# Kernel tuning notes

Hardware: AMD Instinct MI355X
Metric: run time of the kernel (lower is better)

The kernel has to match this reference:

```python
import jax, jax.numpy as jnp
import numpy as np

B, S, H, D = 8, 2048, 16, 64  # batch, seq, heads, head_dim
DM = H * D                    # d_model = 1024
W = 4                         # compression window / stride


def setup_inputs() -> dict:
    key = jax.random.key(0)
    ks = jax.random.split(key, 6)
    return {
        "pre_q": jax.random.normal(ks[0], (B, S, H, D), dtype=jnp.float32),
        "pre_k": jax.random.normal(ks[1], (B, S, H, D), dtype=jnp.float32),
        "pre_v": jax.random.normal(ks[2], (B, S, H, D), dtype=jnp.float32),
        "k_conv_kernel": jax.random.normal(ks[3], (W, D, D), dtype=jnp.float32) * (1.0 / np.sqrt(W * D)),
        "k_conv_bias": jnp.zeros((D,), dtype=jnp.float32),
        "v_conv_kernel": jax.random.normal(ks[4], (W, D, D), dtype=jnp.float32) * (1.0 / np.sqrt(W * D)),
        "v_conv_bias": jnp.zeros((D,), dtype=jnp.float32),
        "output_weights": jax.random.normal(ks[5], (DM, DM), dtype=jnp.float32) * (1.0 / np.sqrt(DM)),
        "compression_window": W,
    }


def _compress(x, kernel, bias, window):
    # x: [B, H, S, D] -> strided valid conv along seq -> [B, H, Sc, D]
    b, h, s, d = x.shape
    x2 = x.reshape(b * h, s, d)  # NWC
    y = jax.lax.conv_general_dilated(
        x2, kernel, window_strides=(window,), padding="VALID",
        dimension_numbers=("NWC", "WIO", "NWC")) + bias
    return y.reshape(b, h, -1, d)


def reference(pre_q, pre_k, pre_v, k_conv_kernel, k_conv_bias,
              v_conv_kernel, v_conv_bias, output_weights, compression_window):
    b, s, h, d = pre_q.shape
    q = jnp.transpose(pre_q, (0, 2, 1, 3))  # [B,H,S,D]
    k = jnp.transpose(pre_k, (0, 2, 1, 3))
    v = jnp.transpose(pre_v, (0, 2, 1, 3))
    kc = _compress(k, k_conv_kernel, k_conv_bias, compression_window)  # [B,H,Sc,D]
    vc = _compress(v, v_conv_kernel, v_conv_bias, compression_window)
    scale = 1.0 / np.sqrt(d).astype(np.float32)
    scores = jnp.einsum("bhsd,bhtd->bhst", q, kc) * scale  # [B,H,S,Sc]
    attn = jax.nn.softmax(scores, axis=-1)
    out = jnp.einsum("bhst,bhtd->bhsd", attn, vc)  # [B,H,S,D]
    out = jnp.transpose(out, (0, 2, 1, 3)).reshape(b, s, h * d)  # [B,S,DM]
    return out @ output_weights  # [B,S,DM]
```

## Files before the change

kernel.cpp:

```cpp
#include <hip/hip_runtime.h>
#include <hip/hip_bf16.h>
#include <math.h>

#define B_   8
#define S_   2048
#define H_   16
#define D_   64
#define DM_  1024
#define W_   4
#define SC_  512

typedef float f32x4 __attribute__((ext_vector_type(4)));
typedef short bf16x8 __attribute__((ext_vector_type(8)));
typedef short bf16x4 __attribute__((ext_vector_type(4)));

static __device__ inline short f2bf(float f) {
    union { float f; unsigned u; } v; v.f = f;
    unsigned r = v.u + 0x7fffu + ((v.u >> 16) & 1u);
    return (short)(r >> 16);
}

static __device__ inline short bfc(float f) {
    __hip_bfloat16 h = __float2bfloat16(f);
    union { __hip_bfloat16 h; short s; } u; u.h = h; return u.s;
}

static __device__ inline float fexp2(float x) {
    float r; asm("v_exp_f32 %0, %1" : "=v"(r) : "v"(x)); return r;
}

static __device__ inline void gll16(const void* g, void* l) {
    __builtin_amdgcn_global_load_lds(
        (const __attribute__((address_space(1))) unsigned int*)g,
        (__attribute__((address_space(3))) unsigned int*)l, 16, 0, 0);
}

__global__ __launch_bounds__(256) void wtrans_kernel(
    const float* __restrict__ Wg, short* __restrict__ Wt)
{
    __shared__ float ws[64][68];
    const int tid = threadIdx.x;
    const int n0 = blockIdx.x * 64, k0 = blockIdx.y * 64;
    #pragma unroll
    for (int i = 0; i < 4; ++i) {
        int idx = i * 256 + tid;
        int row = idx >> 4, c4 = idx & 15;
        float4 v = *(const float4*)(Wg + (size_t)(k0 + row) * 1024 + n0 + c4 * 4);
        *(float4*)(&ws[row][c4 * 4]) = v;
    }
    __syncthreads();
    #pragma unroll
    for (int i = 0; i < 2; ++i) {
        int idx = i * 256 + tid;
        int n = idx >> 3, kc8 = idx & 7;
        bf16x8 o;
        #pragma unroll
        for (int j = 0; j < 8; ++j) o[j] = f2bf(ws[kc8 * 8 + j][n]);
        *(bf16x8*)(Wt + (size_t)(n0 + n) * 1024 + k0 + kc8 * 8) = o;
    }
}

__global__ __launch_bounds__(256) void prep_kernel(
    const float* __restrict__ kk, const float* __restrict__ vk,
    short* __restrict__ BkT)
{
    __shared__ float ws[64][68];
    const int tid = threadIdx.x;
    const int k0 = blockIdx.x * 64;
    const float* src = blockIdx.y ? vk : kk;
    short* dst = BkT + (size_t)blockIdx.y * 64 * 256;
    #pragma unroll
    for (int i = 0; i < 4; ++i) {
        int idx = i * 256 + tid;
        int row = idx >> 4, c4 = idx & 15;
        float4 v = *(const float4*)(src + (size_t)(k0 + row) * 64 + c4 * 4);
        *(float4*)(&ws[row][c4 * 4]) = v;
    }
    __syncthreads();
    #pragma unroll
    for (int i = 0; i < 2; ++i) {
        int idx = i * 256 + tid;
        int n = idx >> 3, kc8 = idx & 7;
        bf16x8 o;
        #pragma unroll
        for (int j = 0; j < 8; ++j) o[j] = f2bf(ws[kc8 * 8 + j][n]);
        *(bf16x8*)(dst + (size_t)n * 256 + k0 + kc8 * 8) = o;
    }
}

template<int TR>
__global__ __launch_bounds__(256) void compress_mfma(
    const float* __restrict__ x,
    const short* __restrict__ bkt,
    const float* __restrict__ bias,
    short* __restrict__ y)
{
    __shared__ __align__(16) char Ah[16384];
    __shared__ __align__(16) char Al[16384];
    __shared__ __align__(16) char Bs[32768];
    const int tid  = threadIdx.x;
    const int bid  = (blockIdx.x & 7) * 256 + (blockIdx.x >> 3);
    const int tile = bid & 15;
    const int bh   = bid >> 4;
    const int h    = bh & 15;
    const int b    = bh >> 4;
    const int t0   = tile * 32;
    const int s0   = t0 * 4;

    #pragma unroll
    for (int i = 0; i < 8; ++i) {
        int idx = i * 256 + tid;
        int sl = idx >> 4, c4 = idx & 15;
        float4 v = *(const float4*)(x + (((size_t)(b * S_ + s0 + sl) * H_ + h) * D_) + c4 * 4);
        int tl = sl >> 2, k = (sl & 3) * 64 + c4 * 4;
        bf16x4 h4, l4;
        #pragma unroll
        for (int j = 0; j < 4; ++j) {
            float f = ((const float*)&v)[j];
            short hs = f2bf(f);
            union { unsigned u; float f; } hf; hf.u = ((unsigned)(unsigned short)hs) << 16;
            h4[j] = hs;
            l4[j] = f2bf(f - hf.f);
        }
        int base = (tl * 256 + k) * 2;
        int sw = (tl & 7) << 4;
        *(bf16x4*)(Ah + (base ^ sw)) = h4;
        *(bf16x4*)(Al + (base ^ sw)) = l4;
    }
    #pragma unroll
    for (int i = 0; i < 8; ++i) {
        int idx = i * 256 + tid;
        int dr = idx >> 5, part = idx & 31;
        bf16x8 bv = *(const bf16x8*)(bkt + dr * 256 + part * 8);
        *(bf16x8*)(Bs + ((dr * 512 + part * 16) ^ ((dr & 7) << 4))) = bv;
    }

    const int w = tid >> 6, ln = tid & 63, ln15 = ln & 15, hi = ln >> 4;
    const int wm = w & 1, wn = w >> 1;
    f32x4 acc[2];
    #pragma unroll
    for (int nf = 0; nf < 2; ++nf) {
        float bv = bias[wn * 32 + nf * 16 + ln15];
        acc[nf] = (f32x4){bv, bv, bv, bv};
    }
    __syncthreads();

    const int arow = wm * 16 + ln15;
    const int asw  = (arow & 7) << 4;
    #pragma unroll
    for (int kst = 0; kst < 16; ++kst) {
        const char* Asel = (kst < 8) ? Ah : Al;
        int kb = (kst & 7) * 64 + hi * 16;
        bf16x8 af = *(const bf16x8*)(Asel + ((arow * 512 + kb) ^ asw));
        #pragma unroll
        for (int nf = 0; nf < 2; ++nf) {
            int br = wn * 32 + nf * 16 + ln15;
            bf16x8 b8 = *(const bf16x8*)(Bs + ((br * 512 + kb) ^ ((br & 7) << 4)));
            acc[nf] = __builtin_amdgcn_mfma_f32_16x16x32_bf16(af, b8, acc[nf], 0, 0, 0);
        }
    }

    #pragma unroll
    for (int nf = 0; nf < 2; ++nf) {
        int dout = wn * 32 + nf * 16 + ln15;
        #pragma unroll
        for (int r = 0; r < 4; ++r) {
            float vv = acc[nf][r];
            if (!TR) {
                int t = t0 + wm * 16 + hi * 4 + r;
                y[((size_t)bh * SC_ + t) * 64 + dout] = f2bf(vv);
            } else {
                int p = r + 4 * wm + 8 * hi;
                y[((size_t)bh * 64 + dout) * SC_ + t0 + p] = f2bf(vv);
            }
        }
    }
}

__global__ __launch_bounds__(1024) void attn_kernel(
    const float* __restrict__ q,
    const short* __restrict__ kc,
    const short* __restrict__ vct,
    short* __restrict__ xb)
{
    __shared__ __align__(16) char klds[32768];
    __shared__ __align__(16) char vlds[32768];

    const int tid  = threadIdx.x;
    const int bid  = (blockIdx.x & 7) * 128 + (blockIdx.x >> 3);
    const int qc   = bid & 7;
    const int bh   = bid >> 3;
    const int h    = bh & 15;
    const int b    = bh >> 4;
    const int w    = tid >> 6;
    const int ln   = tid & 63;
    const int ln15 = ln & 15;
    const int hi   = ln >> 4;
    const int sbase = qc * 256 + w * 16;
    const int swz  = (ln15 & 7) << 4;

    const short* kg = kc + (size_t)bh * SC_ * 64;
    const short* vg = vct + (size_t)bh * 64 * SC_;

    const int krow = tid >> 3, kpart = tid & 7;
    const int vrow = tid >> 5, vpart = tid & 31;

    bf16x8 qb[2];
    {
        const float qs = 0.18033688011112042f;
        const float* qrow = q + (((size_t)(b * S_ + sbase + ln15)) * H_ + h) * D_;
        #pragma unroll
        for (int dblk = 0; dblk < 2; ++dblk) {
            const float* p = qrow + dblk * 32 + hi * 8;
            #pragma unroll
            for (int j = 0; j < 8; ++j) qb[dblk][j] = bfc(p[j] * qs);
        }
    }

    const char* kp0 = klds + ln15 * 128 + ((hi * 16) ^ swz);
    const char* kp1 = klds + ln15 * 128 + ((64 + hi * 16) ^ swz);
    const char* vp0 = vlds + ln15 * 512 + ((hi * 16) ^ swz);
    const char* vp1 = vlds + ln15 * 512 + ((64 + hi * 16) ^ swz);

    f32x4 oa[4];
    #pragma unroll
    for (int ns = 0; ns < 4; ++ns) oa[ns] = (f32x4){0.f, 0.f, 0.f, 0.f};
    float lrun = 0.f;

    #pragma unroll
    for (int ph = 0; ph < 2; ++ph) {
        if (ph) __syncthreads();
        #pragma unroll
        for (int i = 0; i < 2; ++i) {
            int row = krow + i * 128;
            bf16x8 kv = *(const bf16x8*)(kg + (ph * 256 + row) * 64 + kpart * 8);
            *(bf16x8*)(klds + ((row * 128 + kpart * 16) ^ ((row & 7) << 4))) = kv;
        }
        #pragma unroll
        for (int i = 0; i < 2; ++i) {
            int row = vrow + i * 32;
            bf16x8 vv = *(const bf16x8*)(vg + (size_t)row * SC_ + ph * 256 + vpart * 8);
            *(bf16x8*)(vlds + ((row * 512 + vpart * 16) ^ ((row & 7) << 4))) = vv;
        }
        __syncthreads();

        #pragma unroll
        for (int kt = 0; kt < 4; ++kt) {
            f32x4 d[4];
            __builtin_amdgcn_s_setprio(1);
            #pragma unroll
            for (int ks = 0; ks < 4; ++ks) {
                bf16x8 ka0 = *(const bf16x8*)(kp0 + kt * 8192 + ks * 2048);
                bf16x8 ka1 = *(const bf16x8*)(kp1 + kt * 8192 + ks * 2048);
                d[ks] = __builtin_amdgcn_mfma_f32_16x16x32_bf16(ka0, qb[0], (f32x4){0.f,0.f,0.f,0.f}, 0, 0, 0);
                d[ks] = __builtin_amdgcn_mfma_f32_16x16x32_bf16(ka1, qb[1], d[ks], 0, 0, 0);
            }
            __builtin_amdgcn_s_setprio(0);

            bf16x8 pa[2];
            #pragma unroll
            for (int ks = 0; ks < 4; ++ks)
                #pragma unroll
                for (int r = 0; r < 4; ++r) {
                    float e = fexp2(d[ks][r]);
                    lrun += e;
                    pa[ks >> 1][(ks & 1) * 4 + r] = bfc(e);
                }

            __builtin_amdgcn_s_setprio(1);
            #pragma unroll
            for (int ns = 0; ns < 4; ++ns) {
                bf16x8 vb0 = *(const bf16x8*)(vp0 + ns * 8192 + kt * 128);
                bf16x8 vb1 = *(const bf16x8*)(vp1 + ns * 8192 + kt * 128);
                oa[ns] = __builtin_amdgcn_mfma_f32_16x16x32_bf16(pa[0], vb0, oa[ns], 0, 0, 0);
                oa[ns] = __builtin_amdgcn_mfma_f32_16x16x32_bf16(pa[1], vb1, oa[ns], 0, 0, 0);
            }
            __builtin_amdgcn_s_setprio(0);
        }
    }

    lrun += __shfl_xor(lrun, 16);
    lrun += __shfl_xor(lrun, 32);
    float li[4];
    #pragma unroll
    for (int r = 0; r < 4; ++r) li[r] = 1.f / __shfl(lrun, hi * 4 + r);
    #pragma unroll
    for (int ns = 0; ns < 4; ++ns)
        #pragma unroll
        for (int r = 0; r < 4; ++r) {
            size_t i0 = ((size_t)(b * S_ + sbase + hi * 4 + r)) * DM_ + h * 64 + ns * 16 + ln15;
            xb[i0] = f2bf(oa[ns][r] * li[r]);
        }
}

__global__ __launch_bounds__(256) void proj_kernel(
    const short* __restrict__ Xb,
    const short* __restrict__ Wt,
    float* __restrict__ out)
{
    __shared__ __align__(16) short As[128 * 64];
    __shared__ __align__(16) short Bs[128 * 64];
    const int tid  = threadIdx.x;
    const int wid  = tid >> 6;
    const int ln   = tid & 63;
    const int ln15 = ln & 15;
    const int hi   = ln >> 4;
    const int wr   = wid >> 1, wc = wid & 1;
    const int bid  = (blockIdx.x & 7) * 128 + (blockIdx.x >> 3);
    const int tn   = bid & 7, tm = bid >> 3;
    const int m0   = tm * 128, n0 = tn * 128;
    const int spart = tid & 7;

    f32x4 acc[4][4];
    #pragma unroll
    for (int i = 0; i < 4; ++i)
        #pragma unroll
        for (int j = 0; j < 4; ++j) acc[i][j] = (f32x4){0.f, 0.f, 0.f, 0.f};

    for (int k0 = 0; k0 < 1024; k0 += 64) {
        #pragma unroll
        for (int i = 0; i < 4; ++i) {
            int row = (i * 256 + tid) >> 3;
            int ldsoff = __builtin_amdgcn_readfirstlane((i * 256 + (tid & ~63)) * 16);
            gll16(Xb + (size_t)(m0 + row) * 1024 + k0 + spart * 8, (char*)As + ldsoff);
            gll16(Wt + (size_t)(n0 + row) * 1024 + k0 + spart * 8, (char*)Bs + ldsoff);
        }
        __syncthreads();

        #pragma unroll
        for (int ks = 0; ks < 2; ++ks) {
            bf16x8 af[4], bfr[4];
            #pragma unroll
            for (int mf = 0; mf < 4; ++mf)
                af[mf] = *(const bf16x8*)((const char*)As + (wr * 64 + mf * 16 + ln15) * 128 + ks * 64 + hi * 16);
            #pragma unroll
            for (int nf = 0; nf < 4; ++nf)
                bfr[nf] = *(const bf16x8*)((const char*)Bs + (wc * 64 + nf * 16 + ln15) * 128 + ks * 64 + hi * 16);
            #pragma unroll
            for (int mf = 0; mf < 4; ++mf)
                #pragma unroll
                for (int nf = 0; nf < 4; ++nf)
                    acc[mf][nf] = __builtin_amdgcn_mfma_f32_16x16x32_bf16(af[mf], bfr[nf], acc[mf][nf], 0, 0, 0);
        }
        __syncthreads();
    }

    #pragma unroll
    for (int mf = 0; mf < 4; ++mf)
        #pragma unroll
        for (int nf = 0; nf < 4; ++nf)
            #pragma unroll
            for (int r = 0; r < 4; ++r)
                out[(size_t)(m0 + wr * 64 + mf * 16 + hi * 4 + r) * 1024 + n0 + wc * 64 + nf * 16 + ln15] =
                    acc[mf][nf][r];
}

extern "C" void kernel_launch(void* const* d_in, const int* in_sizes, int n_in,
                              void* d_out, int out_size, void* d_ws, size_t ws_size,
                              hipStream_t stream) {
    const float* pre_q = (const float*)d_in[0];
    const float* pre_k = (const float*)d_in[1];
    const float* pre_v = (const float*)d_in[2];
    const float* kkern = (const float*)d_in[3];
    const float* kbias = (const float*)d_in[4];
    const float* vkern = (const float*)d_in[5];
    const float* vbias = (const float*)d_in[6];
    const float* wout  = (const float*)d_in[7];
    float* out = (float*)d_out;

    short* Xb  = (short*)d_ws;
    short* kcb = Xb + (size_t)(B_ * S_) * DM_;
    short* vct = kcb + (size_t)B_ * H_ * SC_ * D_;
    short* Wtb = vct + (size_t)B_ * H_ * SC_ * D_;
    short* BkT = Wtb + (size_t)DM_ * DM_;

    prep_kernel<<<dim3(4, 2), 256, 0, stream>>>(kkern, vkern, BkT);
    wtrans_kernel<<<dim3(16, 16), 256, 0, stream>>>(wout, Wtb);
    compress_mfma<0><<<B_ * H_ * 16, 256, 0, stream>>>(pre_k, BkT, kbias, kcb);
    compress_mfma<1><<<B_ * H_ * 16, 256, 0, stream>>>(pre_v, BkT + 64 * 256, vbias, vct);
    attn_kernel<<<B_ * H_ * (S_ / 256), 1024, 0, stream>>>(pre_q, kcb, vct, Xb);
    proj_kernel<<<DM_ / 128 * ((B_ * S_) / 128), 256, 0, stream>>>(Xb, Wtb, out);
}
```

Baseline: 169.2 us.

## Pre-pack K/V into MFMA fragment order and double-buffer projection GEMM

Adds a repack kernel that writes compressed K and V into per-lane MFMA fragment order. This lets the attention kernel load operands straight from global memory (through cache) without LDS staging or barriers, using smaller 256-thread blocks over 64 query rows. The projection GEMM switches to double-buffered LDS so the next tile's global loads overlap the current tile's MFMAs. The cost is an extra kernel launch, an extra pass over the K/V data, and attention operand reads served from L2 instead of LDS.

```diff
diff --git a/kernel.cpp b/kernel.cpp
--- a/kernel.cpp
+++ b/kernel.cpp
@@ -177,33 +177,42 @@
     }
 }
 
-__global__ __launch_bounds__(1024) void attn_kernel(
+__global__ __launch_bounds__(512) void repack_kernel(
+    const short* __restrict__ kc, const short* __restrict__ vct,
+    short* __restrict__ kfrag, short* __restrict__ vfrag)
+{
+    const int tid  = threadIdx.x;
+    const int kt   = blockIdx.x & 7;
+    const int bh   = blockIdx.x >> 3;
+    const int ln15 = tid & 15;
+    const int hi   = (tid >> 4) & 3;
+    const int sel  = tid >> 7;
+    const int half = (tid >> 6) & 1;
+
+    bf16x8 kv = *(const bf16x8*)(kc + ((size_t)bh * 512 + kt * 64 + sel * 16 + ln15) * 64 + half * 32 + hi * 8);
+    *(bf16x8*)(kfrag + ((size_t)(bh * 8 + kt) * 512 + tid) * 8) = kv;
+
+    bf16x8 vv = *(const bf16x8*)(vct + ((size_t)bh * 64 + sel * 16 + ln15) * 512 + kt * 64 + half * 32 + hi * 8);
+    *(bf16x8*)(vfrag + ((size_t)(bh * 8 + kt) * 512 + tid) * 8) = vv;
+}
+
+__global__ __launch_bounds__(256) void attn_kernel(
     const float* __restrict__ q,
-    const short* __restrict__ kc,
-    const short* __restrict__ vct,
+    const short* __restrict__ kfrag,
+    const short* __restrict__ vfrag,
     short* __restrict__ xb)
 {
-    __shared__ __align__(16) char klds[32768];
-    __shared__ __align__(16) char vlds[32768];
-
     const int tid  = threadIdx.x;
-    const int bid  = (blockIdx.x & 7) * 128 + (blockIdx.x >> 3);
-    const int qc   = bid & 7;
-    const int bh   = bid >> 3;
+    const int bid  = (blockIdx.x & 7) * 512 + (blockIdx.x >> 3);
+    const int qc   = bid & 31;
+    const int bh   = bid >> 5;
     const int h    = bh & 15;
     const int b    = bh >> 4;
     const int w    = tid >> 6;
     const int ln   = tid & 63;
     const int ln15 = ln & 15;
     const int hi   = ln >> 4;
-    const int sbase = qc * 256 + w * 16;
-    const int swz  = (ln15 & 7) << 4;
-
-    const short* kg = kc + (size_t)bh * SC_ * 64;
-    const short* vg = vct + (size_t)bh * 64 * SC_;
-
-    const int krow = tid >> 3, kpart = tid & 7;
-    const int vrow = tid >> 5, vpart = tid & 31;
+    const int sbase = qc * 64 + w * 16;
 
     bf16x8 qb[2];
     {
@@ -217,68 +226,59 @@
         }
     }
 
-    const char* kp0 = klds + ln15 * 128 + ((hi * 16) ^ swz);
-    const char* kp1 = klds + ln15 * 128 + ((64 + hi * 16) ^ swz);
-    const char* vp0 = vlds + ln15 * 512 + ((hi * 16) ^ swz);
-    const char* vp1 = vlds + ln15 * 512 + ((64 + hi * 16) ^ swz);
+    const short* kfb = kfrag + (size_t)bh * 32768 + ln * 8;
+    const short* vfb = vfrag + (size_t)bh * 32768 + ln * 8;
 
     f32x4 oa[4];
     #pragma unroll
     for (int ns = 0; ns < 4; ++ns) oa[ns] = (f32x4){0.f, 0.f, 0.f, 0.f};
-    float lrun = 0.f;
-
-    #pragma unroll
-    for (int ph = 0; ph < 2; ++ph) {
-        if (ph) __syncthreads();
-        #pragma unroll
-        for (int i = 0; i < 2; ++i) {
-            int row = krow + i * 128;
-            bf16x8 kv = *(const bf16x8*)(kg + (ph * 256 + row) * 64 + kpart * 8);
-            *(bf16x8*)(klds + ((row * 128 + kpart * 16) ^ ((row & 7) << 4))) = kv;
-        }
-        #pragma unroll
-        for (int i = 0; i < 2; ++i) {
-            int row = vrow + i * 32;
-            bf16x8 vv = *(const bf16x8*)(vg + (size_t)row * SC_ + ph * 256 + vpart * 8);
-            *(bf16x8*)(vlds + ((row * 512 + vpart * 16) ^ ((row & 7) << 4))) = vv;
-        }
-        __syncthreads();
-
-        #pragma unroll
-        for (int kt = 0; kt < 4; ++kt) {
-            f32x4 d[4];
-            __builtin_amdgcn_s_setprio(1);
-            #pragma unroll
-            for (int ks = 0; ks < 4; ++ks) {
-                bf16x8 ka0 = *(const bf16x8*)(kp0 + kt * 8192 + ks * 2048);
-                bf16x8 ka1 = *(const bf16x8*)(kp1 + kt * 8192 + ks * 2048);
-                d[ks] = __builtin_amdgcn_mfma_f32_16x16x32_bf16(ka0, qb[0], (f32x4){0.f,0.f,0.f,0.f}, 0, 0, 0);
-                d[ks] = __builtin_amdgcn_mfma_f32_16x16x32_bf16(ka1, qb[1], d[ks], 0, 0, 0);
+    float lr[4] = {0.f, 0.f, 0.f, 0.f};
+
+    #pragma unroll
+    for (int kt = 0; kt < 8; ++kt) {
+        bf16x8 ka[4][2];
+        #pragma unroll
+        for (int ks = 0; ks < 4; ++ks)
+            #pragma unroll
+            for (int dblk = 0; dblk < 2; ++dblk)
+                ka[ks][dblk] = *(const bf16x8*)(kfb + (kt * 8 + ks * 2 + dblk) * 512);
+
+        f32x4 d[4];
+        __builtin_amdgcn_s_setprio(1);
+        #pragma unroll
+        for (int ks = 0; ks < 4; ++ks) {
+            d[ks] = __builtin_amdgcn_mfma_f32_16x16x32_bf16(ka[ks][0], qb[0], (f32x4){0.f,0.f,0.f,0.f}, 0, 0, 0);
+            d[ks] = __builtin_amdgcn_mfma_f32_16x16x32_bf16(ka[ks][1], qb[1], d[ks], 0, 0, 0);
+        }
+        __builtin_amdgcn_s_setprio(0);
+
+        bf16x8 pa[2];
+        #pragma unroll
+        for (int ks = 0; ks < 4; ++ks)
+            #pragma unroll
+            for (int r = 0; r < 4; ++r) {
+                float e = fexp2(d[ks][r]);
+                lr[ks] += e;
+                pa[ks >> 1][(ks & 1) * 4 + r] = bfc(e);
             }
-            __builtin_amdgcn_s_setprio(0);
-
-            bf16x8 pa[2];
-            #pragma unroll
-            for (int ks = 0; ks < 4; ++ks)
-                #pragma unroll
-                for (int r = 0; r < 4; ++r) {
-                    float e = fexp2(d[ks][r]);
-                    lrun += e;
-                    pa[ks >> 1][(ks & 1) * 4 + r] = bfc(e);
-                }
-
-            __builtin_amdgcn_s_setprio(1);
-            #pragma unroll
-            for (int ns = 0; ns < 4; ++ns) {
-                bf16x8 vb0 = *(const bf16x8*)(vp0 + ns * 8192 + kt * 128);
-                bf16x8 vb1 = *(const bf16x8*)(vp1 + ns * 8192 + kt * 128);
-                oa[ns] = __builtin_amdgcn_mfma_f32_16x16x32_bf16(pa[0], vb0, oa[ns], 0, 0, 0);
-                oa[ns] = __builtin_amdgcn_mfma_f32_16x16x32_bf16(pa[1], vb1, oa[ns], 0, 0, 0);
-            }
-            __builtin_amdgcn_s_setprio(0);
-        }
-    }
-
+
+        bf16x8 vb[4][2];
+        #pragma unroll
+        for (int ns = 0; ns < 4; ++ns)
+            #pragma unroll
+            for (int kb = 0; kb < 2; ++kb)
+                vb[ns][kb] = *(const bf16x8*)(vfb + (kt * 8 + ns * 2 + kb) * 512);
+
+        __builtin_amdgcn_s_setprio(1);
+        #pragma unroll
+        for (int ns = 0; ns < 4; ++ns) {
+            oa[ns] = __builtin_amdgcn_mfma_f32_16x16x32_bf16(pa[0], vb[ns][0], oa[ns], 0, 0, 0);
+            oa[ns] = __builtin_amdgcn_mfma_f32_16x16x32_bf16(pa[1], vb[ns][1], oa[ns], 0, 0, 0);
+        }
+        __builtin_amdgcn_s_setprio(0);
+    }
+
+    float lrun = (lr[0] + lr[1]) + (lr[2] + lr[3]);
     lrun += __shfl_xor(lrun, 16);
     lrun += __shfl_xor(lrun, 32);
     float li[4];
@@ -298,8 +298,10 @@
     const short* __restrict__ Wt,
     float* __restrict__ out)
 {
-    __shared__ __align__(16) short As[128 * 64];
-    __shared__ __align__(16) short Bs[128 * 64];
+    __shared__ __align__(16) short As0[128 * 64];
+    __shared__ __align__(16) short Bs0[128 * 64];
+    __shared__ __align__(16) short As1[128 * 64];
+    __shared__ __align__(16) short Bs1[128 * 64];
     const int tid  = threadIdx.x;
     const int wid  = tid >> 6;
     const int ln   = tid & 63;
@@ -317,31 +319,44 @@
         #pragma unroll
         for (int j = 0; j < 4; ++j) acc[i][j] = (f32x4){0.f, 0.f, 0.f, 0.f};
 
-    for (int k0 = 0; k0 < 1024; k0 += 64) {
+    auto stage = [&](short* A, short* B, int k0) {
         #pragma unroll
         for (int i = 0; i < 4; ++i) {
             int row = (i * 256 + tid) >> 3;
             int ldsoff = __builtin_amdgcn_readfirstlane((i * 256 + (tid & ~63)) * 16);
-            gll16(Xb + (size_t)(m0 + row) * 1024 + k0 + spart * 8, (char*)As + ldsoff);
-            gll16(Wt + (size_t)(n0 + row) * 1024 + k0 + spart * 8, (char*)Bs + ldsoff);
-        }
-        __syncthreads();
-
+            gll16(Xb + (size_t)(m0 + row) * 1024 + k0 + spart * 8, (char*)A + ldsoff);
+            gll16(Wt + (size_t)(n0 + row) * 1024 + k0 + spart * 8, (char*)B + ldsoff);
+        }
+    };
+    auto compute = [&](const short* A, const short* B) {
         #pragma unroll
         for (int ks = 0; ks < 2; ++ks) {
             bf16x8 af[4], bfr[4];
             #pragma unroll
             for (int mf = 0; mf < 4; ++mf)
-                af[mf] = *(const bf16x8*)((const char*)As + (wr * 64 + mf * 16 + ln15) * 128 + ks * 64 + hi * 16);
+                af[mf] = *(const bf16x8*)((const char*)A + (wr * 64 + mf * 16 + ln15) * 128 + ks * 64 + hi * 16);
             #pragma unroll
             for (int nf = 0; nf < 4; ++nf)
-                bfr[nf] = *(const bf16x8*)((const char*)Bs + (wc * 64 + nf * 16 + ln15) * 128 + ks * 64 + hi * 16);
+                bfr[nf] = *(const bf16x8*)((const char*)B + (wc * 64 + nf * 16 + ln15) * 128 + ks * 64 + hi * 16);
             #pragma unroll
             for (int mf = 0; mf < 4; ++mf)
                 #pragma unroll
                 for (int nf = 0; nf < 4; ++nf)
                     acc[mf][nf] = __builtin_amdgcn_mfma_f32_16x16x32_bf16(af[mf], bfr[nf], acc[mf][nf], 0, 0, 0);
         }
+    };
+
+    stage(As0, Bs0, 0);
+    __syncthreads();
+
+    #pragma unroll
+    for (int k0 = 0; k0 < 1024; k0 += 128) {
+        stage(As1, Bs1, k0 + 64);
+        compute(As0, Bs0);
+        __syncthreads();
+        if (k0 + 128 < 1024)
+            stage(As0, Bs0, k0 + 128);
+        compute(As1, Bs1);
         __syncthreads();
     }
 
@@ -368,16 +383,19 @@
     const float* wout  = (const float*)d_in[7];
     float* out = (float*)d_out;
 
-    short* Xb  = (short*)d_ws;
-    short* kcb = Xb + (size_t)(B_ * S_) * DM_;
-    short* vct = kcb + (size_t)B_ * H_ * SC_ * D_;
-    short* Wtb = vct + (size_t)B_ * H_ * SC_ * D_;
-    short* BkT = Wtb + (size_t)DM_ * DM_;
+    short* Xb    = (short*)d_ws;
+    short* kcb   = Xb + (size_t)(B_ * S_) * DM_;
+    short* vct   = kcb + (size_t)B_ * H_ * SC_ * D_;
+    short* Wtb   = vct + (size_t)B_ * H_ * SC_ * D_;
+    short* BkT   = Wtb + (size_t)DM_ * DM_;
+    short* kfrag = BkT + 2 * 64 * 256;
+    short* vfrag = kfrag + (size_t)B_ * H_ * SC_ * D_;
 
     prep_kernel<<<dim3(4, 2), 256, 0, stream>>>(kkern, vkern, BkT);
     wtrans_kernel<<<dim3(16, 16), 256, 0, stream>>>(wout, Wtb);
     compress_mfma<0><<<B_ * H_ * 16, 256, 0, stream>>>(pre_k, BkT, kbias, kcb);
     compress_mfma<1><<<B_ * H_ * 16, 256, 0, stream>>>(pre_v, BkT + 64 * 256, vbias, vct);
-    attn_kernel<<<B_ * H_ * (S_ / 256), 1024, 0, stream>>>(pre_q, kcb, vct, Xb);
+    repack_kernel<<<B_ * H_ * 8, 512, 0, stream>>>(kcb, vct, kfrag, vfrag);
+    attn_kernel<<<B_ * H_ * (S_ / 64), 256, 0, stream>>>(pre_q, kfrag, vfrag, Xb);
     proj_kernel<<<DM_ / 128 * ((B_ * S_) / 128), 256, 0, stream>>>(Xb, Wtb, out);
 }
```

After: 201.7 us. 1.19x slower.
